# Optimization experiments

Hardware: AMD Instinct MI355X
Metric: run time of the kernel (lower is better)

The kernel has to match this reference:

```python
import jax, jax.numpy as jnp
from jax import lax
import numpy as np

B, C, H, W, R = 8, 256, 88, 88, 8
EPS = 1e-5

def _conv(x, w, b, stride=1, pad=0):
    out = lax.conv_general_dilated(x, w, (stride, stride), ((pad, pad), (pad, pad)),
                                   dimension_numbers=('NCHW', 'OIHW', 'NCHW'))
    return out + b[None, :, None, None]

def _bn(x, g, b, m, v):
    # eval-mode BatchNorm2d with running stats
    inv = g * lax.rsqrt(v + EPS)
    return (x - m[None, :, None, None]) * inv[None, :, None, None] + b[None, :, None, None]

def _ln_ch(x, g, b):
    # LayerNorm over the channel dim of an NCHW tensor (torch permutes to NHWC, LN, permute back)
    m = x.mean(axis=1, keepdims=True)
    var = ((x - m) ** 2).mean(axis=1, keepdims=True)
    return (x - m) * lax.rsqrt(var + EPS) * g[None, :, None, None] + b[None, :, None, None]

def _sra(qf, kvf, qw, qb, kw, kb, vw, vb, srw, srb, lng, lnb):
    # SpatialReductionAttention with reduction_ratio R > 1
    Bq, Cq, Hq, Wq = qf.shape
    Q = _conv(qf, qw, qb).reshape(Bq, Cq // 8, Hq * Wq)          # (B, C/8, N)
    kvr = _ln_ch(_conv(kvf, srw, srb, stride=R), lng, lnb)        # (B, C, H/R, W/R)
    K = _conv(kvr, kw, kb).reshape(Bq, Cq // 8, -1)               # (B, C/8, Nr)
    V = _conv(kvr, vw, vb).reshape(Bq, Cq, -1)                    # (B, C, Nr)
    scale = (Cq // 8) ** -0.5
    attn = jax.nn.softmax(jnp.einsum('bcn,bcm->bnm', Q, K) * scale, axis=-1)  # (B, N, Nr)
    return jnp.einsum('bcm,bnm->bcn', V, attn).reshape(Bq, Cq, Hq, Wq)


def setup_inputs() -> dict:
    key = jax.random.key(0)
    ks = iter(jax.random.split(key, 64))
    def nrm(shape, s=0.05):
        return jax.random.normal(next(ks), shape, dtype=jnp.float32) * s
    d = {}
    d['f_rgb'] = nrm((B, C, H, W), 1.0)
    d['f_depth'] = nrm((B, C, H, W), 1.0)
    Ct = 2 * C
    d['sm_w1'] = nrm((Ct // 2, Ct, 3, 3)); d['sm_b1'] = jnp.zeros((Ct // 2,))
    d['sm_g1'] = jnp.ones((Ct // 2,)); d['sm_be1'] = jnp.zeros((Ct // 2,))
    d['sm_m1'] = jnp.zeros((Ct // 2,)); d['sm_v1'] = jnp.ones((Ct // 2,))
    d['sm_w2'] = nrm((1, Ct // 2, 1, 1)); d['sm_b2'] = jnp.zeros((1,))
    for pfx in ('d2r', 'r2d'):
        d[pfx + '_q_w'] = nrm((C // 8, C, 1, 1)); d[pfx + '_q_b'] = jnp.zeros((C // 8,))
        d[pfx + '_k_w'] = nrm((C // 8, C, 1, 1)); d[pfx + '_k_b'] = jnp.zeros((C // 8,))
        d[pfx + '_v_w'] = nrm((C, C, 1, 1)); d[pfx + '_v_b'] = jnp.zeros((C,))
        d[pfx + '_sr_w'] = nrm((C, C, R, R), 0.02); d[pfx + '_sr_b'] = jnp.zeros((C,))
        d[pfx + '_ln_g'] = jnp.ones((C,)); d[pfx + '_ln_b'] = jnp.zeros((C,))
        d[pfx + '_norm_g'] = jnp.ones((C,)); d[pfx + '_norm_b'] = jnp.zeros((C,))
    d['d2r_gamma'] = jnp.full((1,), 0.1, dtype=jnp.float32)
    d['r2d_gamma'] = jnp.full((1,), 0.1, dtype=jnp.float32)
    Cf = 2 * C + 1
    d['fus_w'] = nrm((C, Cf, 3, 3)); d['fus_b'] = jnp.zeros((C,))
    d['fus_g'] = jnp.ones((C,)); d['fus_be'] = jnp.zeros((C,))
    d['fus_m'] = jnp.zeros((C,)); d['fus_v'] = jnp.ones((C,))
    return d


def reference(f_rgb, f_depth,
              sm_w1, sm_b1, sm_g1, sm_be1, sm_m1, sm_v1, sm_w2, sm_b2,
              d2r_q_w, d2r_q_b, d2r_k_w, d2r_k_b, d2r_v_w, d2r_v_b,
              d2r_sr_w, d2r_sr_b, d2r_ln_g, d2r_ln_b, d2r_norm_g, d2r_norm_b,
              r2d_q_w, r2d_q_b, r2d_k_w, r2d_k_b, r2d_v_w, r2d_v_b,
              r2d_sr_w, r2d_sr_b, r2d_ln_g, r2d_ln_b, r2d_norm_g, r2d_norm_b,
              d2r_gamma, r2d_gamma,
              fus_w, fus_b, fus_g, fus_be, fus_m, fus_v):
    # align_depth is Identity (depth_channels == rgb_channels), same spatial size
    concat = jnp.concatenate([f_rgb, f_depth], axis=1)
    h1 = jax.nn.relu(_bn(_conv(concat, sm_w1, sm_b1, pad=1), sm_g1, sm_be1, sm_m1, sm_v1))
    spatial_mask = jax.nn.sigmoid(_conv(h1, sm_w2, sm_b2))            # (B, 1, H, W)
    f_depth_masked = f_depth * spatial_mask

    out_d2r = _sra(f_rgb, f_depth_masked, d2r_q_w, d2r_q_b, d2r_k_w, d2r_k_b,
                   d2r_v_w, d2r_v_b, d2r_sr_w, d2r_sr_b, d2r_ln_g, d2r_ln_b)
    out_d2r = _ln_ch(out_d2r, d2r_norm_g, d2r_norm_b)
    f_rgb_enh = f_rgb + jnp.clip(d2r_gamma, 0.0, 1.0) * out_d2r

    out_r2d = _sra(f_depth_masked, f_rgb, r2d_q_w, r2d_q_b, r2d_k_w, r2d_k_b,
                   r2d_v_w, r2d_v_b, r2d_sr_w, r2d_sr_b, r2d_ln_g, r2d_ln_b)
    out_r2d = _ln_ch(out_r2d, r2d_norm_g, r2d_norm_b)
    f_depth_enh = f_depth + jnp.clip(r2d_gamma, 0.0, 1.0) * out_r2d

    fus_in = jnp.concatenate([f_rgb_enh, f_depth_enh, spatial_mask], axis=1)
    return jax.nn.relu(_bn(_conv(fus_in, fus_w, fus_b, pad=1), fus_g, fus_be, fus_m, fus_v))
```

## Files before the change

kernel.cpp:

```cpp
#include <hip/hip_runtime.h>
#include <hip/hip_bf16.h>


typedef __bf16 bf16x8 __attribute__((ext_vector_type(8)));
typedef float f32x4 __attribute__((ext_vector_type(4)));

#define AS1 __attribute__((address_space(1)))
#define AS3 __attribute__((address_space(3)))
#define DEVI __device__ __forceinline__

DEVI float bf2f(unsigned short u){
  union { unsigned int i; float f; } v; v.i = ((unsigned int)u) << 16; return v.f;
}
DEVI unsigned short f2bf(float f){
  union { float f; unsigned int i; } v; v.f = f;
  unsigned int x = v.i;
  unsigned int r = (x + 0x7fffu + ((x >> 16) & 1u)) >> 16;
  return (unsigned short)r;
}

__global__ void bnprep_k(const float* __restrict__ g1, const float* __restrict__ be1,
                         const float* __restrict__ m1, const float* __restrict__ v1,
                         const float* __restrict__ b1,
                         const float* __restrict__ gf, const float* __restrict__ bef,
                         const float* __restrict__ mf, const float* __restrict__ vf,
                         const float* __restrict__ bf,
                         float* __restrict__ sc1, float* __restrict__ sh1,
                         float* __restrict__ scf, float* __restrict__ shf)
{
  int c = threadIdx.x;
  float s = g1[c] * rsqrtf(v1[c] + 1e-5f);
  sc1[c] = s; sh1[c] = (b1[c] - m1[c]) * s + be1[c];
  s = gf[c] * rsqrtf(vf[c] + 1e-5f);
  scf[c] = s; shf[c] = (bf[c] - mf[c]) * s + bef[c];
}

__global__ __launch_bounds__(128)
void zero_border_k(unsigned short* __restrict__ buf, int px_el)
{
  int bi = blockIdx.x;
  int img = bi / 356, e = bi - img * 356;
  int y, x;
  if (e < 90){ y = 0; x = e; }
  else if (e < 180){ y = 89; x = e - 90; }
  else if (e < 268){ y = e - 180 + 1; x = 0; }
  else { y = e - 268 + 1; x = 89; }
  size_t pix = ((size_t)img * 90 + y) * 90 + x;
  int t = threadIdx.x;
  if (t < (px_el >> 3))
    *reinterpret_cast<uint4*>(buf + pix * px_el + t * 8) = uint4{0, 0, 0, 0};
}
__global__ __launch_bounds__(256)
void zero_fustail_k(unsigned short* __restrict__ FusPad)
{
  int idx = blockIdx.x * 256 + threadIdx.x;
  int n = idx >> 3, ch = idx & 7;
  int b = n / 7744, s = n - b * 7744;
  int y = s / 88, x = s - y * 88;
  size_t pix = ((size_t)(b * 90 + y + 1)) * 90 + (x + 1);
  *reinterpret_cast<uint4*>(FusPad + pix * 576 + 512 + ch * 8) = uint4{0, 0, 0, 0};
}

__global__ __launch_bounds__(256)
void prep_xpad_k(const float* __restrict__ rgb, const float* __restrict__ dep,
                 unsigned short* __restrict__ Xpad)
{
  __shared__ unsigned short tile[64][65];
  int bi = blockIdx.x;
  int b = bi / 968;
  int rem = bi - b * 968;
  int cblk = rem / 121;
  int pblk = rem - cblk * 121;
  int t = threadIdx.x;
  int pl = t & 63;
  #pragma unroll
  for (int pass = 0; pass < 16; ++pass){
    int cl = pass * 4 + (t >> 6);
    int c = cblk * 64 + cl;
    const float* sp = (c < 256) ? (rgb + ((size_t)b * 256 + c) * 7744)
                                : (dep + ((size_t)b * 256 + (c - 256)) * 7744);
    tile[cl][pl] = f2bf(sp[pblk * 64 + pl]);
  }
  __syncthreads();
  int cl2 = t & 63;
  for (int pass = 0; pass < 16; ++pass){
    int pl2 = pass * 4 + (t >> 6);
    int pixg = pblk * 64 + pl2;
    int y = pixg / 88, x = pixg - y * 88;
    Xpad[(((size_t)b * 90 + y + 1) * 90 + (x + 1)) * 512 + cblk * 64 + cl2] = tile[cl2][pl2];
  }
}

__global__ __launch_bounds__(256)
void prep_w1t_k(const float* __restrict__ w, unsigned short* __restrict__ o)
{
  int co = blockIdx.x, t = threadIdx.x;
  const float* src = w + (size_t)co * 4608 + t * 18;
  unsigned int* op = (unsigned int*)o;
  #pragma unroll
  for (int k = 0; k < 9; ++k){
    unsigned short lo = f2bf(src[k]);
    unsigned short hi = f2bf(src[9 + k]);
    op[((size_t)k * 256 + co) * 256 + t] = lo | ((unsigned int)hi << 16);
  }
}
__global__ __launch_bounds__(256)
void prep_wfus_k(const float* __restrict__ w, unsigned short* __restrict__ o)
{
  int co = blockIdx.x, t = threadIdx.x;
  const float* src = w + (size_t)co * 4617 + t * 18;
  unsigned int* op = (unsigned int*)o;
  #pragma unroll
  for (int k = 0; k < 9; ++k){
    unsigned short lo = f2bf(src[k]);
    unsigned short hi = f2bf(src[9 + k]);
    op[((size_t)k * 256 + co) * 288 + t] = lo | ((unsigned int)hi << 16);
  }
  if (t < 32){
    #pragma unroll
    for (int k = 0; k < 9; ++k){
      unsigned int val = 0;
      if (t == 0) val = (unsigned int)f2bf(w[(size_t)co * 4617 + 512 * 9 + k]);
      op[((size_t)k * 256 + co) * 288 + 256 + t] = val;
    }
  }
}
__global__ __launch_bounds__(256)
void prep_wsr_k(const float* __restrict__ w, unsigned short* __restrict__ o)
{
  __shared__ float ld[64][65];
  int co = blockIdx.x;
  int t = threadIdx.x;
  for (int cib = 0; cib < 256; cib += 64){
    int cil = t >> 2, tq = t & 3;
    const float* src = w + ((size_t)co * 256 + cib + cil) * 64 + tq * 16;
    float v[16];
    #pragma unroll
    for (int k = 0; k < 16; ++k) v[k] = src[k];
    __syncthreads();
    #pragma unroll
    for (int k = 0; k < 16; ++k) ld[cil][tq * 16 + k] = v[k];
    __syncthreads();
    #pragma unroll
    for (int tp = 0; tp < 16; ++tp){
      int tap = tp * 4 + (t >> 6);
      int ci = t & 63;
      o[((size_t)tap * 256 + co) * 256 + cib + ci] = f2bf(ld[ci][tap]);
    }
  }
}
__global__ __launch_bounds__(256)
void tranw_k(const float* __restrict__ in, unsigned short* __restrict__ out, int R, int C)
{
  __shared__ float tl[32][33];
  int tiles_c = C >> 5;
  int tr = (blockIdx.x / tiles_c) << 5, tc = (blockIdx.x % tiles_c) << 5;
  int t = threadIdx.x; int r = t >> 5, c = t & 31;
  #pragma unroll
  for (int p = 0; p < 4; ++p)
    tl[r + p * 8][c] = in[(size_t)(tr + r + p * 8) * C + tc + c];
  __syncthreads();
  #pragma unroll
  for (int p = 0; p < 4; ++p)
    out[(size_t)(tc + r + p * 8) * R + tr + c] = f2bf(tl[c][r + p * 8]);
}
__global__ __launch_bounds__(256)
void wqprep_k(const float* __restrict__ w, unsigned short* __restrict__ o)
{
  int co = blockIdx.x, t = threadIdx.x;
  int c = t >> 3, e = t & 7;
  o[co * 256 + ((c ^ (co & 7)) * 8) + e] = f2bf(w[co * 256 + t]);
}

struct GemmP {
  const unsigned short* A;
  const unsigned short* W;
  const float* ep_scale;
  const float* ep_shift;
  void* out;
  int img_px, row_px, px_el, ch_off, y0, x0;
  int tapw, stridepix, out_w, out_imgpx;
  int Cin, Mtot, Mtiles, Ntiles, k_per;
};

template<int EPI>
__global__ __launch_bounds__(256)
void gemm_k(GemmP p)
{
  __shared__ __bf16 As[2][128 * 64];
  __shared__ __bf16 Bs[2][128 * 64];
  const int t = threadIdx.x;
  const int lane = t & 63;
  const int wid = t >> 6;
  const int wr = wid >> 1, wc = wid & 1;

  const int cpx = gridDim.x >> 3;
  int pid = (blockIdx.x & 7) * cpx + (blockIdx.x >> 3);
  const int mn = p.Mtiles * p.Ntiles;
  int within = pid % mn;
  int slot = pid / mn;
  int mt = within / p.Ntiles;
  int nt = within - mt * p.Ntiles;
  int kb = slot * p.k_per;
  int tap0 = kb / p.Cin;
  int ntap = p.k_per / p.Cin;

  long long apix[4]; int cbg8[4]; int wrow[4];
  #pragma unroll
  for (int i = 0; i < 4; ++i){
    int r = i * 32 + (t >> 3);
    cbg8[i] = ((t & 7) ^ (r & 7)) * 8;
    int n = mt * 128 + r;
    int nc = n < p.Mtot ? n : 0;
    int b = nc / p.out_imgpx; int rr = nc - b * p.out_imgpx;
    int yo = rr / p.out_w;    int xo = rr - yo * p.out_w;
    apix[i] = (long long)b * p.img_px + (long long)(yo * p.stridepix + p.y0) * p.row_px
            + (xo * p.stridepix + p.x0);
    wrow[i] = (nt * 128 + r) * p.Cin + cbg8[i];
  }

  f32x4 acc[4][4];
  #pragma unroll
  for (int i = 0; i < 4; ++i)
    #pragma unroll
    for (int j = 0; j < 4; ++j)
      acc[i][j] = f32x4{0.f, 0.f, 0.f, 0.f};

  const long long wstap = 256LL * p.Cin;

  auto STAGE = [&](int buf, int tap, int cib){
    int dy = tap / p.tapw, dx = tap - dy * p.tapw;
    const unsigned short* wb = p.W + (long long)tap * wstap + cib;
    const long long aoff = (long long)(dy * p.row_px + dx) * p.px_el + p.ch_off + cib;
    #pragma unroll
    for (int i = 0; i < 4; ++i){
      __builtin_amdgcn_global_load_lds(
          (AS1 void*)(p.A + apix[i] * p.px_el + aoff + cbg8[i]),
          (AS3 void*)(&As[buf][i * 2048 + wid * 512]),
          16, 0, 0);
      __builtin_amdgcn_global_load_lds(
          (AS1 void*)(wb + wrow[i]),
          (AS3 void*)(&Bs[buf][i * 2048 + wid * 512]),
          16, 0, 0);
    }
  };

  const int NT = (p.Cin >> 6) * ntap;
  STAGE(0, tap0, 0);
  int tpn = 1, tap_n = tap0 + 1, cib_n = 0;
  int cur = 0;

  for (int kt = 0; kt < NT; ++kt){
    if (kt + 1 < NT){
      STAGE(cur ^ 1, tap_n, cib_n);
      ++tpn; ++tap_n;
      if (tpn == ntap){ tpn = 0; tap_n = tap0; cib_n += 64; }
      asm volatile("s_waitcnt vmcnt(8)" ::: "memory");
    } else {
      asm volatile("s_waitcnt vmcnt(0)" ::: "memory");
    }
    __builtin_amdgcn_s_barrier();
    __builtin_amdgcn_sched_barrier(0);

    #pragma unroll
    for (int ks = 0; ks < 2; ++ks){
      bf16x8 av[4], bv[4];
      #pragma unroll
      for (int mi = 0; mi < 4; ++mi){
        int ar = wr * 64 + mi * 16 + (lane & 15);
        int cb = (ks * 4 + (lane >> 4)) ^ (ar & 7);
        av[mi] = *reinterpret_cast<const bf16x8*>(&As[cur][ar * 64 + cb * 8]);
      }
      #pragma unroll
      for (int ni = 0; ni < 4; ++ni){
        int br = wc * 64 + ni * 16 + (lane & 15);
        int cb = (ks * 4 + (lane >> 4)) ^ (br & 7);
        bv[ni] = *reinterpret_cast<const bf16x8*>(&Bs[cur][br * 64 + cb * 8]);
      }
      #pragma unroll
      for (int mi = 0; mi < 4; ++mi)
        #pragma unroll
        for (int ni = 0; ni < 4; ++ni)
          acc[mi][ni] = __builtin_amdgcn_mfma_f32_16x16x32_bf16(av[mi], bv[ni], acc[mi][ni], 0, 0, 0);
    }

    __builtin_amdgcn_sched_barrier(0);
    __builtin_amdgcn_s_barrier();
    cur ^= 1;
  }

  const int r0 = (lane >> 4) * 4;
  const int c0 = lane & 15;
  #pragma unroll
  for (int mi = 0; mi < 4; ++mi){
    int nbase = mt * 128 + wr * 64 + mi * 16 + r0;
    #pragma unroll
    for (int ni = 0; ni < 4; ++ni){
      int co = nt * 128 + wc * 64 + ni * 16 + c0;
      f32x4 a = acc[mi][ni];
      if constexpr (EPI == 0){
        float sc = p.ep_scale[co], sh = p.ep_shift[co];
        unsigned short* o = (unsigned short*)p.out;
        #pragma unroll
        for (int r = 0; r < 4; ++r){
          float v = fmaf(a[r], sc, sh); v = v > 0.f ? v : 0.f;
          o[(size_t)(nbase + r) * 256 + co] = f2bf(v);
        }
      } else if constexpr (EPI == 1){
        float sc = p.ep_scale[co], sh = p.ep_shift[co];
        float* o = (float*)p.out;
        int b = nbase / 7744; int s = nbase - b * 7744;
        float4 v;
        v.x = fmaxf(fmaf(a[0], sc, sh), 0.f);
        v.y = fmaxf(fmaf(a[1], sc, sh), 0.f);
        v.z = fmaxf(fmaf(a[2], sc, sh), 0.f);
        v.w = fmaxf(fmaf(a[3], sc, sh), 0.f);
        *reinterpret_cast<float4*>(o + ((size_t)(b * 256 + co)) * 7744 + s) = v;
      } else {
        float* o = (float*)p.out + (size_t)slot * 968 * 256;
        #pragma unroll
        for (int r = 0; r < 4; ++r){
          int n = nbase + r;
          if (n < p.Mtot) o[(size_t)n * 256 + co] = a[r];
        }
      }
    }
  }
}

__global__ __launch_bounds__(256)
void mask_k(const unsigned short* __restrict__ h1, const float* __restrict__ w2,
            const float* __restrict__ b2, float* __restrict__ mask,
            unsigned short* __restrict__ FusPad)
{
  __shared__ float w[256];
  int t = threadIdx.x;
  w[t] = w2[t];
  __syncthreads();
  int n = blockIdx.x * 256 + t;
  const unsigned short* row = h1 + (size_t)n * 256;
  float s = b2[0];
  for (int c = 0; c < 256; c += 8){
    union { uint4 v; unsigned short s_[8]; } u;
    u.v = *reinterpret_cast<const uint4*>(row + c);
    #pragma unroll
    for (int j = 0; j < 8; ++j) s = fmaf(bf2f(u.s_[j]), w[c + j], s);
  }
  float m = 1.f / (1.f + __expf(-s));
  mask[n] = m;
  int b = n / 7744, sr = n - b * 7744;
  int y = sr / 88, x = sr - y * 88;
  FusPad[(((size_t)b * 90 + y + 1) * 90 + (x + 1)) * 576 + 512] = f2bf(m);
}

__global__ __launch_bounds__(256)
void fdm_k(const unsigned short* __restrict__ Xpad, const float* __restrict__ mask,
           unsigned short* __restrict__ fdm)
{
  int idx = blockIdx.x * 256 + threadIdx.x;
  int n = idx >> 5, cb = idx & 31;
  int b = n / 7744, s = n - b * 7744;
  int y = s / 88, x = s - y * 88;
  size_t pix = ((size_t)(b * 90 + y + 1)) * 90 + x + 1;
  union { uint4 v; unsigned short s_[8]; } u, w;
  u.v = *reinterpret_cast<const uint4*>(Xpad + pix * 512 + 256 + cb * 8);
  float m = mask[n];
  #pragma unroll
  for (int j = 0; j < 8; ++j) w.s_[j] = f2bf(bf2f(u.s_[j]) * m);
  *reinterpret_cast<uint4*>(fdm + (size_t)n * 256 + cb * 8) = w.v;
}

__global__ __launch_bounds__(256)
void lnkvr_k(const float* __restrict__ part, const float* __restrict__ srb,
             const float* __restrict__ lng, const float* __restrict__ lnb,
             unsigned short* __restrict__ kvr)
{
  int n = blockIdx.x, t = threadIdx.x;
  float v = srb[t];
  for (int s = 0; s < 16; ++s) v += part[((size_t)s * 968 + n) * 256 + t];
  float s1 = v, s2 = v * v;
  #pragma unroll
  for (int o = 1; o < 64; o <<= 1){ s1 += __shfl_xor(s1, o, 64); s2 += __shfl_xor(s2, o, 64); }
  __shared__ float a1[4], a2[4];
  if ((t & 63) == 0){ a1[t >> 6] = s1; a2[t >> 6] = s2; }
  __syncthreads();
  float t1 = a1[0] + a1[1] + a1[2] + a1[3];
  float t2 = a2[0] + a2[1] + a2[2] + a2[3];
  float mean = t1 * (1.f / 256.f);
  float var = t2 * (1.f / 256.f) - mean * mean;
  float rstd = rsqrtf(var + 1e-5f);
  kvr[(size_t)n * 256 + t] = f2bf((v - mean) * rstd * lng[t] + lnb[t]);
}

__global__ __launch_bounds__(256)
void dotconv_k(const unsigned short* __restrict__ src,
               const unsigned short* __restrict__ wt, const float* __restrict__ bias,
               float* __restrict__ out)
{
  __shared__ unsigned short wl[256 * 32];
  const int t = threadIdx.x;
  {
    uint4* d = (uint4*)wl; const uint4* s = (const uint4*)wt;
    #pragma unroll
    for (int k = 0; k < 4; ++k) d[t + 256 * k] = s[t + 256 * k];
  }
  __syncthreads();
  const int n = blockIdx.x * 8 + (t >> 5);
  const int co = t & 31;
  const unsigned short* row = src + (size_t)n * 256;
  float sum = bias[co];
  for (int c = 0; c < 256; c += 8){
    union { uint4 v; unsigned short s_[8]; } u;
    u.v = *reinterpret_cast<const uint4*>(row + c);
    #pragma unroll
    for (int j = 0; j < 8; ++j)
      sum = fmaf(bf2f(u.s_[j]), bf2f(wl[(c + j) * 32 + co]), sum);
  }
  out[(size_t)n * 32 + co] = sum;
}

__global__ __launch_bounds__(256)
void vconv_k(const unsigned short* __restrict__ kvr, const unsigned short* __restrict__ vwt,
             const float* __restrict__ vb, unsigned short* __restrict__ VBt)
{
  __shared__ float rowf[256];
  const int n = blockIdx.x, t = threadIdx.x;
  rowf[t] = bf2f(kvr[(size_t)n * 256 + t]);
  __syncthreads();
  float sum = vb[t];
  #pragma unroll 8
  for (int c = 0; c < 256; ++c)
    sum = fmaf(rowf[c], bf2f(vwt[(size_t)c * 256 + t]), sum);
  int b = n / 121, m = n - b * 121;
  VBt[(size_t)b * 32768 + (size_t)t * 128 + m] = f2bf(sum);
}

__global__ __launch_bounds__(512, 2)
void attn_k(const unsigned short* __restrict__ Qsrc, int qmode,
            const unsigned short* __restrict__ wq, const float* __restrict__ qb,
            const float* __restrict__ Kbuf,
            const unsigned short* __restrict__ VBt,
            const unsigned short* __restrict__ Xpad, int resChOff,
            unsigned short* __restrict__ FusPad, int outChOff,
            const float* __restrict__ ng, const float* __restrict__ nbv,
            const float* __restrict__ gammap)
{
  __shared__ unsigned short Vt[2][256][64];
  __shared__ unsigned short Pl[2][128][64];
  __shared__ unsigned short Qs[128][64];
  __shared__ unsigned short Ks[128][64];
  __shared__ unsigned short Wqs[32][256];

  const int t = threadIdx.x;
  const int lane = t & 63;
  const int w = t >> 6;
  const int c15 = lane & 15;
  const int h = lane >> 4;

  const int bid = blockIdx.x;
  const int b = bid / 61;
  const int rb = bid - b * 61;
  const int nb0 = rb * 128;

  const unsigned short* vsrc = VBt + (size_t)b * 32768;
  #pragma unroll
  for (int kt = 0; kt < 2; ++kt)
    #pragma unroll
    for (int i = 0; i < 4; ++i){
      int rowbase = i * 64 + w * 8;
      int c = rowbase + (lane >> 3);
      int mchunk = (lane & 7) ^ (c & 7);
      __builtin_amdgcn_global_load_lds(
        (AS1 void*)(vsrc + (size_t)c * 128 + kt * 64 + mchunk * 8),
        (AS3 void*)(&Vt[kt][rowbase][0]),
        16, 0, 0);
    }

  {
    uint4* d = (uint4*)&Wqs[0][0]; const uint4* s = (const uint4*)wq;
    d[t] = s[t];
    d[t + 512] = s[t + 512];
  }
  {
    int m = t >> 2, part = t & 3;
    union { uint4 v; unsigned short s_[8]; } u;
    u.v = uint4{0, 0, 0, 0};
    if (m < 121){
      const float* kp = Kbuf + ((size_t)b * 121 + m) * 32 + part * 8;
      float4 a = *reinterpret_cast<const float4*>(kp);
      float4 bb = *reinterpret_cast<const float4*>(kp + 4);
      u.s_[0] = f2bf(a.x); u.s_[1] = f2bf(a.y); u.s_[2] = f2bf(a.z); u.s_[3] = f2bf(a.w);
      u.s_[4] = f2bf(bb.x); u.s_[5] = f2bf(bb.y); u.s_[6] = f2bf(bb.z); u.s_[7] = f2bf(bb.w);
    }
    *reinterpret_cast<uint4*>(&Ks[m][(part ^ (m & 7)) * 8]) = u.v;
  }
  __syncthreads();

  const int nA = w * 16 + c15;
  const float scale = 0.17677669529663687f;

  {
    int gn = nb0 + nA; if (gn > 7743) gn = 7743;
    const unsigned short* xrow;
    if (qmode){
      int y = gn / 88, x = gn - y * 88;
      xrow = Qsrc + (((size_t)(b * 90) + y + 1) * 90 + (x + 1)) * 512;
    } else {
      xrow = Qsrc + ((size_t)b * 7744 + gn) * 256;
    }
    f32x4 qacc[2];
    qacc[0] = f32x4{0.f, 0.f, 0.f, 0.f};
    qacc[1] = f32x4{0.f, 0.f, 0.f, 0.f};
    #pragma unroll
    for (int kt = 0; kt < 8; ++kt){
      bf16x8 ax = *reinterpret_cast<const bf16x8*>(xrow + kt * 32 + h * 8);
      #pragma unroll
      for (int ni = 0; ni < 2; ++ni){
        int co = ni * 16 + c15;
        bf16x8 bw = *reinterpret_cast<const bf16x8*>(&Wqs[co][((kt * 4 + h) ^ (co & 7)) * 8]);
        qacc[ni] = __builtin_amdgcn_mfma_f32_16x16x32_bf16(ax, bw, qacc[ni], 0, 0, 0);
      }
    }
    #pragma unroll
    for (int ni = 0; ni < 2; ++ni){
      int co = ni * 16 + c15;
      float bq = qb[co];
      #pragma unroll
      for (int r = 0; r < 4; ++r){
        int n = w * 16 + 4 * h + r;
        int chunk = (co >> 3) ^ (n & 7);
        Qs[n][chunk * 8 + (co & 7)] = f2bf((qacc[ni][r] + bq) * scale);
      }
    }
  }

  bf16x8 aq = *reinterpret_cast<const bf16x8*>(&Qs[nA][(h ^ (nA & 7)) * 8]);
  f32x4 sv[8];
  #pragma unroll
  for (int ni = 0; ni < 8; ++ni){
    int mrow = ni * 16 + c15;
    bf16x8 bk = *reinterpret_cast<const bf16x8*>(&Ks[mrow][(h ^ (mrow & 7)) * 8]);
    sv[ni] = __builtin_amdgcn_mfma_f32_16x16x32_bf16(aq, bk, f32x4{0.f,0.f,0.f,0.f}, 0, 0, 0);
  }
  if (c15 >= 9) sv[7] = f32x4{-1e30f, -1e30f, -1e30f, -1e30f};

  float rden[4];
  #pragma unroll
  for (int r = 0; r < 4; ++r){
    float mx = sv[0][r];
    #pragma unroll
    for (int ni = 1; ni < 8; ++ni) mx = fmaxf(mx, sv[ni][r]);
    #pragma unroll
    for (int o = 1; o < 16; o <<= 1) mx = fmaxf(mx, __shfl_xor(mx, o, 64));
    float sm = 0.f;
    #pragma unroll
    for (int ni = 0; ni < 8; ++ni){
      float p = __expf(sv[ni][r] - mx);
      sv[ni][r] = p;
      sm += p;
    }
    #pragma unroll
    for (int o = 1; o < 16; o <<= 1) sm += __shfl_xor(sm, o, 64);
    rden[r] = 1.f / sm;
  }
  #pragma unroll
  for (int ni = 0; ni < 8; ++ni){
    int m = ni * 16 + c15;
    int kt = m >> 6;
    int mq = (m & 63) >> 3;
    #pragma unroll
    for (int r = 0; r < 4; ++r){
      int n = w * 16 + 4 * h + r;
      Pl[kt][n][(mq ^ (n & 7)) * 8 + (m & 7)] = f2bf(sv[ni][r] * rden[r]);
    }
  }

  bf16x8 pa[2][2];
  #pragma unroll
  for (int kt = 0; kt < 2; ++kt)
    #pragma unroll
    for (int ks = 0; ks < 2; ++ks)
      pa[kt][ks] = *reinterpret_cast<const bf16x8*>(&Pl[kt][nA][((ks * 4 + h) ^ (nA & 7)) * 8]);

  f32x4 acc[16];
  #pragma unroll
  for (int ni = 0; ni < 16; ++ni) acc[ni] = f32x4{0.f, 0.f, 0.f, 0.f};
  #pragma unroll
  for (int ni = 0; ni < 16; ++ni){
    int crow = ni * 16 + c15;
    #pragma unroll
    for (int kt = 0; kt < 2; ++kt)
      #pragma unroll
      for (int ks = 0; ks < 2; ++ks){
        bf16x8 bv = *reinterpret_cast<const bf16x8*>(&Vt[kt][crow][((ks * 4 + h) ^ (crow & 7)) * 8]);
        acc[ni] = __builtin_amdgcn_mfma_f32_16x16x32_bf16(pa[kt][ks], bv, acc[ni], 0, 0, 0);
      }
  }

  float ngv[16], nbb[16];
  #pragma unroll
  for (int ni = 0; ni < 16; ++ni){
    int c = ni * 16 + c15;
    ngv[ni] = ng[c]; nbb[ni] = nbv[c];
  }
  float g = gammap[0]; g = fminf(fmaxf(g, 0.f), 1.f);

  #pragma unroll
  for (int r = 0; r < 4; ++r){
    float s1 = 0.f, s2 = 0.f;
    #pragma unroll
    for (int ni = 0; ni < 16; ++ni){ float v = acc[ni][r]; s1 += v; s2 += v * v; }
    #pragma unroll
    for (int o = 1; o < 16; o <<= 1){ s1 += __shfl_xor(s1, o, 64); s2 += __shfl_xor(s2, o, 64); }
    float mean = s1 * (1.f / 256.f);
    float var = s2 * (1.f / 256.f) - mean * mean;
    float rstd = rsqrtf(var + 1e-5f);

    int nloc = w * 16 + 4 * h + r;
    int rix = nb0 + nloc;
    if (rix < 7744){
      int y = rix / 88, x = rix - y * 88;
      size_t pix = ((size_t)(b * 90) + y + 1) * 90 + (x + 1);
      const unsigned short* res = Xpad + pix * 512 + resChOff;
      unsigned short* outp = FusPad + pix * 576 + outChOff;
      #pragma unroll
      for (int ni = 0; ni < 16; ++ni){
        int c = ni * 16 + c15;
        float yv = (acc[ni][r] - mean) * rstd * ngv[ni] + nbb[ni];
        outp[c] = f2bf(bf2f(res[c]) + g * yv);
      }
    }
  }
}

extern "C" void kernel_launch(void* const* d_in, const int* in_sizes, int n_in,
                              void* d_out, int out_size, void* d_ws, size_t ws_size,
                              hipStream_t stream)
{
  const float* P[42];
  for (int i = 0; i < 42; ++i) P[i] = (const float*)d_in[i];

  char* ws = (char*)d_ws;
  size_t off = 0;
  auto take = [&](size_t bytes) -> char* {
    char* p = ws + off; off += (bytes + 255) & ~(size_t)255; return p;
  };
  unsigned short* XPAD = (unsigned short*)take(8ull * 8100 * 512 * 2);
  unsigned short* FUSP = (unsigned short*)take(8ull * 8100 * 576 * 2);
  unsigned short* H1   = (unsigned short*)take(61952ull * 256 * 2);
  unsigned short* FDM  = H1;
  unsigned short* W1T  = (unsigned short*)take(9ull * 256 * 512 * 2);
  unsigned short* WFT  = (unsigned short*)take(9ull * 256 * 576 * 2);
  unsigned short* WSRA = (unsigned short*)take(64ull * 256 * 256 * 2);
  unsigned short* WSRB = (unsigned short*)take(64ull * 256 * 256 * 2);
  float* PART = (float*)take(16ull * 968 * 256 * 4);
  unsigned short* KVR = (unsigned short*)take(968ull * 256 * 2);
  float* KB   = (float*)take(968ull * 32 * 4);
  unsigned short* VBT = (unsigned short*)take(8ull * 256 * 128 * 2);
  float* MASK = (float*)take(61952ull * 4);
  float* SC1 = (float*)take(256 * 4);
  float* SH1 = (float*)take(256 * 4);
  float* SCF = (float*)take(256 * 4);
  float* SHF = (float*)take(256 * 4);
  unsigned short* WQSA = (unsigned short*)take(32ull * 256 * 2);
  unsigned short* WQSB = (unsigned short*)take(32ull * 256 * 2);
  unsigned short* KWTA = (unsigned short*)take(256ull * 32 * 2);
  unsigned short* VWTA = (unsigned short*)take(256ull * 256 * 2);
  unsigned short* KWTB = (unsigned short*)take(256ull * 32 * 2);
  unsigned short* VWTB = (unsigned short*)take(256ull * 256 * 2);
  (void)ws_size; (void)in_sizes; (void)n_in; (void)out_size;

  zero_border_k<<<8 * 356, 128, 0, stream>>>(XPAD, 512);
  zero_border_k<<<8 * 356, 128, 0, stream>>>(FUSP, 576);
  zero_fustail_k<<<1936, 256, 0, stream>>>(FUSP);
  hipMemsetAsync(VBT, 0, 8ull * 256 * 128 * 2, stream);

  bnprep_k<<<1, 256, 0, stream>>>(P[4], P[5], P[6], P[7], P[3],
                                  P[38], P[39], P[40], P[41], P[37],
                                  SC1, SH1, SCF, SHF);
  prep_xpad_k<<<7744, 256, 0, stream>>>(P[0], P[1], XPAD);
  prep_w1t_k<<<256, 256, 0, stream>>>(P[2], W1T);
  prep_wfus_k<<<256, 256, 0, stream>>>(P[36], WFT);
  prep_wsr_k<<<256, 256, 0, stream>>>(P[16], WSRA);
  prep_wsr_k<<<256, 256, 0, stream>>>(P[28], WSRB);
  wqprep_k<<<32, 256, 0, stream>>>(P[10], WQSA);
  wqprep_k<<<32, 256, 0, stream>>>(P[22], WQSB);
  tranw_k<<<8, 256, 0, stream>>>(P[12], KWTA, 32, 256);
  tranw_k<<<64, 256, 0, stream>>>(P[14], VWTA, 256, 256);
  tranw_k<<<8, 256, 0, stream>>>(P[24], KWTB, 32, 256);
  tranw_k<<<64, 256, 0, stream>>>(P[26], VWTB, 256, 256);

  GemmP g1{};
  g1.A = XPAD; g1.W = W1T; g1.ep_scale = SC1; g1.ep_shift = SH1; g1.out = H1;
  g1.img_px = 8100; g1.row_px = 90; g1.px_el = 512; g1.ch_off = 0; g1.y0 = 0; g1.x0 = 0;
  g1.tapw = 3; g1.stridepix = 1; g1.out_w = 88; g1.out_imgpx = 7744;
  g1.Cin = 512; g1.Mtot = 61952; g1.Mtiles = 484; g1.Ntiles = 2; g1.k_per = 4608;
  gemm_k<0><<<968, 256, 0, stream>>>(g1);

  mask_k<<<242, 256, 0, stream>>>(H1, P[8], P[9], MASK, FUSP);
  fdm_k<<<7744, 256, 0, stream>>>(XPAD, MASK, FDM);

  GemmP gs{};
  gs.A = FDM; gs.W = WSRA; gs.out = PART;
  gs.img_px = 7744; gs.row_px = 88; gs.px_el = 256; gs.ch_off = 0; gs.y0 = 0; gs.x0 = 0;
  gs.tapw = 8; gs.stridepix = 8; gs.out_w = 11; gs.out_imgpx = 121;
  gs.Cin = 256; gs.Mtot = 968; gs.Mtiles = 8; gs.Ntiles = 2; gs.k_per = 1024;
  gemm_k<2><<<256, 256, 0, stream>>>(gs);
  lnkvr_k<<<968, 256, 0, stream>>>(PART, P[17], P[18], P[19], KVR);
  dotconv_k<<<121, 256, 0, stream>>>(KVR, KWTA, P[13], KB);
  vconv_k<<<968, 256, 0, stream>>>(KVR, VWTA, P[15], VBT);
  attn_k<<<488, 512, 0, stream>>>(XPAD, 1, WQSA, P[11], KB, VBT, XPAD, 0,
                                  FUSP, 0, P[20], P[21], P[34]);

  gs.A = XPAD; gs.W = WSRB;
  gs.img_px = 8100; gs.row_px = 90; gs.px_el = 512; gs.y0 = 1; gs.x0 = 1;
  gemm_k<2><<<256, 256, 0, stream>>>(gs);
  lnkvr_k<<<968, 256, 0, stream>>>(PART, P[29], P[30], P[31], KVR);
  dotconv_k<<<121, 256, 0, stream>>>(KVR, KWTB, P[25], KB);
  vconv_k<<<968, 256, 0, stream>>>(KVR, VWTB, P[27], VBT);
  attn_k<<<488, 512, 0, stream>>>(FDM, 0, WQSB, P[23], KB, VBT, XPAD, 256,
                                  FUSP, 256, P[32], P[33], P[35]);

  GemmP gf{};
  gf.A = FUSP; gf.W = WFT; gf.ep_scale = SCF; gf.ep_shift = SHF; gf.out = d_out;
  gf.img_px = 8100; gf.row_px = 90; gf.px_el = 576; gf.ch_off = 0; gf.y0 = 0; gf.x0 = 0;
  gf.tapw = 3; gf.stridepix = 1; gf.out_w = 88; gf.out_imgpx = 7744;
  gf.Cin = 576; gf.Mtot = 61952; gf.Mtiles = 484; gf.Ntiles = 2; gf.k_per = 5184;
  gemm_k<1><<<968, 256, 0, stream>>>(gf);
}
```

Before: 599.2 us.

## Add 256x256-tile 512-thread implicit-GEMM kernel for the two 3x3 convs

Adds a new gemm256_k kernel that computes a 256x256 output tile per workgroup of 512 threads, with double-buffered LDS fed by global_load_lds, staggered loads interleaved with MFMA phases, and an XCD-aware tile mapping. The two large 3x3 convolutions (mask branch and fusion) now use it with 242 workgroups, so each workgroup covers all output channels and the input-patch reloads that came from splitting the channels across two tiles go away. The old gemm_k keeps only the partial-sum epilogue. In exchange the kernel needs more registers and LDS per workgroup, and 242 workgroups may leave CUs idle in a tail.

```diff
diff --git a/kernel.cpp b/kernel.cpp
--- a/kernel.cpp
+++ b/kernel.cpp
@@ -8,6 +8,7 @@
 #define AS1 __attribute__((address_space(1)))
 #define AS3 __attribute__((address_space(3)))
 #define DEVI __device__ __forceinline__
+#define BARRIER() do { asm volatile("" ::: "memory"); __builtin_amdgcn_s_barrier(); asm volatile("" ::: "memory"); } while (0)
 
 DEVI float bf2f(unsigned short u){
   union { unsigned int i; float f; } v; v.i = ((unsigned int)u) << 16; return v.f;
@@ -298,6 +299,151 @@
     for (int ni = 0; ni < 4; ++ni){
       int co = nt * 128 + wc * 64 + ni * 16 + c0;
       f32x4 a = acc[mi][ni];
+      float* o = (float*)p.out + (size_t)slot * 968 * 256;
+      #pragma unroll
+      for (int r = 0; r < 4; ++r){
+        int n = nbase + r;
+        if (n < p.Mtot) o[(size_t)n * 256 + co] = a[r];
+      }
+    }
+  }
+}
+
+template<int EPI>
+__global__ __launch_bounds__(512, 2)
+void gemm256_k(GemmP p)
+{
+  __shared__ __bf16 As[2][256 * 64];
+  __shared__ __bf16 Bs[2][256 * 64];
+  const int t = threadIdx.x;
+  const int lane = t & 63;
+  const int w = t >> 6;
+  const int wr = w >> 2, wc = w & 3;
+  const int c15 = lane & 15;
+  const int h = lane >> 4;
+
+  const int nwg = gridDim.x;
+  const int q = nwg >> 3, r8 = nwg & 7;
+  const int bid = blockIdx.x;
+  const int xcd = bid & 7;
+  const int mt = (xcd < r8 ? xcd * (q + 1) : r8 * (q + 1) + (xcd - r8) * q) + (bid >> 3);
+
+  long long apixel[4];
+  const unsigned short* wsrc[4];
+  int lbase[4];
+  #pragma unroll
+  for (int i = 0; i < 4; ++i){
+    int r = i * 64 + (t >> 3);
+    int cb = ((t & 7) ^ (r & 7)) * 8;
+    int n = mt * 256 + r;
+    int b = n / p.out_imgpx; int rr = n - b * p.out_imgpx;
+    int yo = rr / p.out_w;   int xo = rr - yo * p.out_w;
+    long long pix = (long long)b * p.img_px + (long long)(yo * p.stridepix + p.y0) * p.row_px
+                  + (xo * p.stridepix + p.x0);
+    apixel[i] = pix * p.px_el + p.ch_off + cb;
+    wsrc[i] = p.W + (long long)r * p.Cin + cb;
+    lbase[i] = i * 4096 + w * 512;
+  }
+
+  f32x4 acc[8][4];
+  #pragma unroll
+  for (int i = 0; i < 8; ++i)
+    #pragma unroll
+    for (int j = 0; j < 4; ++j)
+      acc[i][j] = f32x4{0.f, 0.f, 0.f, 0.f};
+
+  const long long wstap = 256LL * p.Cin;
+  const int ntap = p.k_per / p.Cin;
+  const int NT = (p.Cin >> 6) * ntap;
+
+  auto STG = [&](int buf, int i, long long aoff, long long woff){
+    __builtin_amdgcn_global_load_lds(
+        (AS1 void*)(p.A + apixel[i] + aoff),
+        (AS3 void*)(&As[buf][lbase[i]]), 16, 0, 0);
+    __builtin_amdgcn_global_load_lds(
+        (AS1 void*)(wsrc[i] + woff),
+        (AS3 void*)(&Bs[buf][lbase[i]]), 16, 0, 0);
+  };
+  auto LDA = [&](bf16x8* av, int mi0, int ks, int buf){
+    #pragma unroll
+    for (int m = 0; m < 4; ++m){
+      int ar = wr * 128 + (mi0 + m) * 16 + c15;
+      int cb = (ks * 4 + h) ^ (ar & 7);
+      av[m] = *reinterpret_cast<const bf16x8*>(&As[buf][ar * 64 + cb * 8]);
+    }
+  };
+  auto LDB = [&](bf16x8* bv, int ks, int buf){
+    #pragma unroll
+    for (int n = 0; n < 4; ++n){
+      int br = wc * 64 + n * 16 + c15;
+      int cb = (ks * 4 + h) ^ (br & 7);
+      bv[n] = *reinterpret_cast<const bf16x8*>(&Bs[buf][br * 64 + cb * 8]);
+    }
+  };
+  auto MM = [&](bf16x8* av, bf16x8* bv, int mi0){
+    __builtin_amdgcn_s_setprio(1);
+    #pragma unroll
+    for (int m = 0; m < 4; ++m)
+      #pragma unroll
+      for (int n = 0; n < 4; ++n)
+        acc[mi0 + m][n] = __builtin_amdgcn_mfma_f32_16x16x32_bf16(av[m], bv[n], acc[mi0 + m][n], 0, 0, 0);
+    __builtin_amdgcn_s_setprio(0);
+  };
+
+  #pragma unroll
+  for (int i = 0; i < 4; ++i) STG(0, i, 0, 0);
+
+  int tap_n = 1, cib_n = 0;
+  int cur = 0;
+
+  for (int kt = 0; kt < NT; ++kt){
+    const bool last = (kt == NT - 1);
+    long long aoff_n = 0, woff_n = 0;
+    if (!last){
+      int dy = tap_n / p.tapw, dx = tap_n - dy * p.tapw;
+      aoff_n = (long long)(dy * p.row_px + dx) * p.px_el + cib_n;
+      woff_n = (long long)tap_n * wstap + cib_n;
+    }
+    bf16x8 av[4], bv[4];
+
+    if (!last){
+      STG(cur ^ 1, 0, aoff_n, woff_n);
+      asm volatile("s_waitcnt vmcnt(2)" ::: "memory");
+    } else {
+      asm volatile("s_waitcnt vmcnt(0)" ::: "memory");
+    }
+    BARRIER();
+    LDA(av, 0, 0, cur); LDB(bv, 0, cur);
+    MM(av, bv, 0);
+    BARRIER();
+    LDA(av, 4, 0, cur);
+    if (!last) STG(cur ^ 1, 1, aoff_n, woff_n);
+    BARRIER();
+    MM(av, bv, 4);
+    BARRIER();
+    LDA(av, 0, 1, cur); LDB(bv, 1, cur);
+    if (!last) STG(cur ^ 1, 2, aoff_n, woff_n);
+    BARRIER();
+    MM(av, bv, 0);
+    BARRIER();
+    LDA(av, 4, 1, cur);
+    if (!last) STG(cur ^ 1, 3, aoff_n, woff_n);
+    BARRIER();
+    MM(av, bv, 4);
+    BARRIER();
+
+    cur ^= 1;
+    if (!last){ ++tap_n; if (tap_n == ntap){ tap_n = 0; cib_n += 64; } }
+  }
+
+  const int r0 = (lane >> 4) * 4;
+  #pragma unroll
+  for (int mi = 0; mi < 8; ++mi){
+    int nbase = mt * 256 + wr * 128 + mi * 16 + r0;
+    #pragma unroll
+    for (int ni = 0; ni < 4; ++ni){
+      int co = wc * 64 + ni * 16 + c15;
+      f32x4 a = acc[mi][ni];
       if constexpr (EPI == 0){
         float sc = p.ep_scale[co], sh = p.ep_shift[co];
         unsigned short* o = (unsigned short*)p.out;
@@ -306,7 +452,7 @@
           float v = fmaf(a[r], sc, sh); v = v > 0.f ? v : 0.f;
           o[(size_t)(nbase + r) * 256 + co] = f2bf(v);
         }
-      } else if constexpr (EPI == 1){
+      } else {
         float sc = p.ep_scale[co], sh = p.ep_shift[co];
         float* o = (float*)p.out;
         int b = nbase / 7744; int s = nbase - b * 7744;
@@ -316,13 +462,6 @@
         v.z = fmaxf(fmaf(a[2], sc, sh), 0.f);
         v.w = fmaxf(fmaf(a[3], sc, sh), 0.f);
         *reinterpret_cast<float4*>(o + ((size_t)(b * 256 + co)) * 7744 + s) = v;
-      } else {
-        float* o = (float*)p.out + (size_t)slot * 968 * 256;
-        #pragma unroll
-        for (int r = 0; r < 4; ++r){
-          int n = nbase + r;
-          if (n < p.Mtot) o[(size_t)n * 256 + co] = a[r];
-        }
       }
     }
   }
@@ -694,8 +833,8 @@
   g1.A = XPAD; g1.W = W1T; g1.ep_scale = SC1; g1.ep_shift = SH1; g1.out = H1;
   g1.img_px = 8100; g1.row_px = 90; g1.px_el = 512; g1.ch_off = 0; g1.y0 = 0; g1.x0 = 0;
   g1.tapw = 3; g1.stridepix = 1; g1.out_w = 88; g1.out_imgpx = 7744;
-  g1.Cin = 512; g1.Mtot = 61952; g1.Mtiles = 484; g1.Ntiles = 2; g1.k_per = 4608;
-  gemm_k<0><<<968, 256, 0, stream>>>(g1);
+  g1.Cin = 512; g1.Mtot = 61952; g1.Mtiles = 242; g1.Ntiles = 1; g1.k_per = 4608;
+  gemm256_k<0><<<242, 512, 0, stream>>>(g1);
 
   mask_k<<<242, 256, 0, stream>>>(H1, P[8], P[9], MASK, FUSP);
   fdm_k<<<7744, 256, 0, stream>>>(XPAD, MASK, FDM);
@@ -725,6 +864,6 @@
   gf.A = FUSP; gf.W = WFT; gf.ep_scale = SCF; gf.ep_shift = SHF; gf.out = d_out;
   gf.img_px = 8100; gf.row_px = 90; gf.px_el = 576; gf.ch_off = 0; gf.y0 = 0; gf.x0 = 0;
   gf.tapw = 3; gf.stridepix = 1; gf.out_w = 88; gf.out_imgpx = 7744;
-  gf.Cin = 576; gf.Mtot = 61952; gf.Mtiles = 484; gf.Ntiles = 2; gf.k_per = 5184;
-  gemm_k<1><<<968, 256, 0, stream>>>(gf);
-}
+  gf.Cin = 576; gf.Mtot = 61952; gf.Mtiles = 242; gf.Ntiles = 1; gf.k_per = 5184;
+  gemm256_k<1><<<242, 512, 0, stream>>>(gf);
+}
```

Result: faster. 552.6 us (-7.8%).
